# Performance work log

Hardware: AMD Instinct MI355X
Metric: run time of the kernel (lower is better)

## Reference

```python
import jax, jax.numpy as jnp
import numpy as np

B, S, D = 2, 2048, 1024
H, DH = 16, 64  # n_heads, d_head; D == H*DH
OUTPUT_SCALE = 1.0
EPS = 1e-08

def setup_inputs() -> dict:
    key = jax.random.key(0)
    k1, k2, k3 = jax.random.split(key, 3)
    x = jax.random.normal(k1, (B, S, D), dtype=jnp.float32)
    # causal-style mask would also work; use all-True [B,S,S] bool mask (True = attend)
    mask = jnp.tril(jnp.ones((S, S), dtype=bool))[None].repeat(B, axis=0)
    Wqkv = jax.random.normal(k2, (D, 3 * D), dtype=jnp.float32) * (1.0 / np.sqrt(D))
    Wo = jax.random.normal(k3, (D, D), dtype=jnp.float32) * (1.0 / np.sqrt(D))
    tau = jnp.full((H, 1, 1), float(DH) ** 0.5, dtype=jnp.float32)  # learned per-head temperature
    return {"x": x, "mask": mask, "Wqkv": Wqkv, "Wo": Wo, "tau": tau}

def reference(x, mask, Wqkv, Wo, tau):
    b, s, d = x.shape
    qkv = x @ Wqkv                                   # [B,S,3D]
    q, k, v = jnp.split(qkv, 3, axis=-1)
    # [B,S,D] -> [B,H,S,DH]
    q = q.reshape(b, s, H, DH).transpose(0, 2, 1, 3)
    k = k.reshape(b, s, H, DH).transpose(0, 2, 1, 3)
    v = v.reshape(b, s, H, DH).transpose(0, 2, 1, 3)
    # L2 normalize Q and K along head dim
    q = q / (jnp.linalg.norm(q, axis=-1, keepdims=True) + EPS)
    k = k / (jnp.linalg.norm(k, axis=-1, keepdims=True) + EPS)
    q = q * tau                                       # per-head learned temperature [H,1,1]
    logits = jnp.einsum('bhqd,bhkd->bhqk', q, k) / jnp.sqrt(jnp.float32(DH))
    m = mask if mask.ndim == 4 else mask[:, None, :, :]
    logits = jnp.where(m, logits, jnp.finfo(logits.dtype).min)
    w = jax.nn.softmax(logits, axis=-1)
    attn = jnp.einsum('bhqk,bhkd->bhqd', w, v)        # [B,H,S,DH]
    attn = attn.transpose(0, 2, 1, 3).reshape(b, s, d)
    return (attn @ Wo) * OUTPUT_SCALE
```

## Files before the change

### kernel.cpp

```cpp
#include <hip/hip_runtime.h>
#include <math.h>

#define BATCH 2
#define SEQ 2048
#define DMODEL 1024
#define NHEAD 16
#define DHEAD 64
#define QKV_COLS (3 * DMODEL)
#define EPS 1e-8f
#define LOG2E 1.44269504f

typedef short bf16x8 __attribute__((ext_vector_type(8)));
typedef float f32x4 __attribute__((ext_vector_type(4)));

static __device__ __forceinline__ unsigned short f2bf(float x) {
  unsigned u = __float_as_uint(x);
  u += 0x7fffu + ((u >> 16) & 1u);
  return (unsigned short)(u >> 16);
}

static __device__ __forceinline__ unsigned pkbf(float lo, float hi) {
  const unsigned ul = __float_as_uint(lo) + 0x8000u;
  const unsigned uh = __float_as_uint(hi) + 0x8000u;
  return __builtin_amdgcn_perm(uh, ul, 0x07060302);
}

static __device__ __forceinline__ void async_ld16(const unsigned short* g,
                                                  unsigned short* l) {
  __builtin_amdgcn_global_load_lds(
      (const __attribute__((address_space(1))) void*)g,
      (__attribute__((address_space(3))) void*)(unsigned int)(unsigned long long)l,
      16, 0, 0);
}

__global__ __launch_bounds__(256) void convert_x_kernel(
    const float* __restrict__ x, unsigned short* __restrict__ xb) {
  const size_t i = ((size_t)blockIdx.x * 256 + threadIdx.x) * 4;
  const float4 a = *(const float4*)(x + i);
  ushort4 r;
  r.x = f2bf(a.x); r.y = f2bf(a.y); r.z = f2bf(a.z); r.w = f2bf(a.w);
  *(ushort4*)(xb + i) = r;
}

__global__ __launch_bounds__(256) void transpose_w2_kernel(
    const float* __restrict__ W0, unsigned short* __restrict__ Wt0,
    const float* __restrict__ W1, unsigned short* __restrict__ Wt1) {
  __shared__ float tile[32][33];
  const int bx = blockIdx.x;
  const float* W;
  unsigned short* Wt;
  int N, n0;
  if (bx < 96) { W = W0; Wt = Wt0; N = QKV_COLS; n0 = bx * 32; }
  else         { W = W1; Wt = Wt1; N = DMODEL;   n0 = (bx - 96) * 32; }
  const int K = DMODEL;
  const int k0 = blockIdx.y * 32;
  const int tx = threadIdx.x, ty = threadIdx.y;
#pragma unroll
  for (int i = 0; i < 4; ++i)
    tile[ty + i * 8][tx] = W[(size_t)(k0 + ty + i * 8) * N + n0 + tx];
  __syncthreads();
#pragma unroll
  for (int i = 0; i < 4; ++i)
    Wt[(size_t)(n0 + ty + i * 8) * K + k0 + tx] = f2bf(tile[tx][ty + i * 8]);
}

__global__ __launch_bounds__(256) void sgemm_bf16_kernel(
    const unsigned short* __restrict__ A, const unsigned short* __restrict__ Bt,
    float* __restrict__ C, int M, int N, int K) {
  __shared__ unsigned short As[2][128 * 32];
  __shared__ unsigned short Bs[2][128 * 32];

  const int t = threadIdx.x;
  const int w = t >> 6;
  const int lane = t & 63;
  const int quad = lane >> 4;
  const int lr = lane & 15;
  const int wr = w >> 1, wc = w & 1;
  const int m0 = blockIdx.y * 128;
  const int n0 = blockIdx.x * 128;

  const int srow = w * 32 + (lane >> 2);
  const int scol = (lane & 3) * 8;
  const unsigned short* ga = A + (size_t)(m0 + srow) * K + scol;
  const unsigned short* gb = Bt + (size_t)(n0 + srow) * K + scol;

  auto stage = [&](int k0, int bb) {
#pragma unroll
    for (int i = 0; i < 2; ++i) {
      async_ld16(ga + (size_t)(i * 16) * K + k0, &As[bb][(w * 32 + i * 16) * 32]);
      async_ld16(gb + (size_t)(i * 16) * K + k0, &Bs[bb][(w * 32 + i * 16) * 32]);
    }
  };

  f32x4 acc[4][4];
  const f32x4 zero4 = {0.f, 0.f, 0.f, 0.f};
#pragma unroll
  for (int i = 0; i < 4; ++i)
#pragma unroll
    for (int j = 0; j < 4; ++j) acc[i][j] = zero4;

  stage(0, 0);
  int bb = 0;
  for (int k0 = 0; k0 < K; k0 += 32, bb ^= 1) {
    __syncthreads();
    if (k0 + 32 < K) stage(k0 + 32, bb ^ 1);

    bf16x8 af[4], bfr[4];
#pragma unroll
    for (int i = 0; i < 4; ++i)
      af[i] = *(const bf16x8*)&As[bb][(wr * 64 + i * 16 + lr) * 32 + quad * 8];
#pragma unroll
    for (int j = 0; j < 4; ++j)
      bfr[j] = *(const bf16x8*)&Bs[bb][(wc * 64 + j * 16 + lr) * 32 + quad * 8];
#pragma unroll
    for (int i = 0; i < 4; ++i)
#pragma unroll
      for (int j = 0; j < 4; ++j)
        acc[i][j] = __builtin_amdgcn_mfma_f32_16x16x32_bf16(af[i], bfr[j], acc[i][j], 0, 0, 0);
  }

#pragma unroll
  for (int i = 0; i < 4; ++i)
#pragma unroll
    for (int r = 0; r < 4; ++r) {
      float* c = C + (size_t)(m0 + wr * 64 + i * 16 + quad * 4 + r) * N + n0 + wc * 64 + lr;
#pragma unroll
      for (int j = 0; j < 4; ++j) c[j * 16] = acc[i][j][r];
    }
}

__global__ __launch_bounds__(256) void qkv_gemm_norm_kernel(
    const unsigned short* __restrict__ A, const unsigned short* __restrict__ Bt,
    const float* __restrict__ tau,
    unsigned short* __restrict__ Qh, unsigned short* __restrict__ Kh,
    unsigned short* __restrict__ Vh) {
  __shared__ unsigned short As[2][128 * 32];
  __shared__ unsigned short Bs[2][128 * 32];

  const int K = DMODEL, N = QKV_COLS;
  const int t = threadIdx.x;
  const int w = t >> 6;
  const int lane = t & 63;
  const int quad = lane >> 4;
  const int lr = lane & 15;
  const int wr = w >> 1, wc = w & 1;
  const int m0 = blockIdx.y * 128;
  const int n0 = blockIdx.x * 128;

  const int srow = w * 32 + (lane >> 2);
  const int scol = (lane & 3) * 8;
  const unsigned short* ga = A + (size_t)(m0 + srow) * K + scol;
  const unsigned short* gb = Bt + (size_t)(n0 + srow) * K + scol;

  auto stage = [&](int k0, int bb) {
#pragma unroll
    for (int i = 0; i < 2; ++i) {
      async_ld16(ga + (size_t)(i * 16) * K + k0, &As[bb][(w * 32 + i * 16) * 32]);
      async_ld16(gb + (size_t)(i * 16) * K + k0, &Bs[bb][(w * 32 + i * 16) * 32]);
    }
  };

  f32x4 acc[4][4];
  const f32x4 zero4 = {0.f, 0.f, 0.f, 0.f};
#pragma unroll
  for (int i = 0; i < 4; ++i)
#pragma unroll
    for (int j = 0; j < 4; ++j) acc[i][j] = zero4;

  stage(0, 0);
  int bb = 0;
  for (int k0 = 0; k0 < K; k0 += 32, bb ^= 1) {
    __syncthreads();
    if (k0 + 32 < K) stage(k0 + 32, bb ^ 1);

    bf16x8 af[4], bfr[4];
#pragma unroll
    for (int i = 0; i < 4; ++i)
      af[i] = *(const bf16x8*)&As[bb][(wr * 64 + i * 16 + lr) * 32 + quad * 8];
#pragma unroll
    for (int j = 0; j < 4; ++j)
      bfr[j] = *(const bf16x8*)&Bs[bb][(wc * 64 + j * 16 + lr) * 32 + quad * 8];
#pragma unroll
    for (int i = 0; i < 4; ++i)
#pragma unroll
      for (int j = 0; j < 4; ++j)
        acc[i][j] = __builtin_amdgcn_mfma_f32_16x16x32_bf16(af[i], bfr[j], acc[i][j], 0, 0, 0);
  }

  const int col0 = n0 + wc * 64;
  const int which = col0 >> 10;
  const int h = (col0 & 1023) >> 6;
  const float tsc = tau[h] * 0.125f * LOG2E;
  unsigned short* dst = (which == 0) ? Qh : (which == 1) ? Kh : Vh;

#pragma unroll
  for (int i = 0; i < 4; ++i)
#pragma unroll
    for (int r = 0; r < 4; ++r) {
      const int s = m0 + wr * 64 + i * 16 + quad * 4 + r;
      unsigned short* ar =
          dst + (((size_t)((s >> 11) * NHEAD + h)) * SEQ + (s & 2047)) * DHEAD;
      float scale;
      if (which == 2) {
        scale = 1.0f;
      } else {
        float ss = 0.f;
#pragma unroll
        for (int j = 0; j < 4; ++j) ss += acc[i][j][r] * acc[i][j][r];
        ss += __shfl_xor(ss, 1, 16);
        ss += __shfl_xor(ss, 2, 16);
        ss += __shfl_xor(ss, 4, 16);
        ss += __shfl_xor(ss, 8, 16);
        scale = 1.0f / (sqrtf(ss) + EPS);
        if (which == 0) scale *= tsc;
      }
#pragma unroll
      for (int j = 0; j < 4; ++j) ar[j * 16 + lr] = f2bf(acc[i][j][r] * scale);
    }
}

__global__ __launch_bounds__(256) void vtrans_kernel(
    const unsigned short* __restrict__ Vh, unsigned short* __restrict__ Vt) {
  __shared__ unsigned short tile[64][72];
  const int bh = blockIdx.x;
  const int s0 = blockIdx.y * 64;
  const int t = threadIdx.x;
  const int sr = t >> 2;
  const int dc = (t & 3) * 16;
  const unsigned short* src = Vh + ((size_t)bh * SEQ + s0 + sr) * DHEAD + dc;
  *(bf16x8*)&tile[sr][dc]     = *(const bf16x8*)(src);
  *(bf16x8*)&tile[sr][dc + 8] = *(const bf16x8*)(src + 8);
  __syncthreads();
  const int dr = t >> 2;
  const int sc = (t & 3) * 16;
  unsigned short buf[16];
#pragma unroll
  for (int i = 0; i < 16; ++i) buf[i] = tile[sc + i][dr];
  unsigned short* dst = Vt + ((size_t)bh * DHEAD + dr) * SEQ + s0 + sc;
  *(bf16x8*)dst       = *(const bf16x8*)buf;
  *(bf16x8*)(dst + 8) = *(const bf16x8*)(buf + 8);
}

#define PLS 72

__global__ __launch_bounds__(256, 2) void attn_kernel(
    const unsigned short* __restrict__ Qh, const unsigned short* __restrict__ Kh,
    const unsigned short* __restrict__ Vt, unsigned short* __restrict__ attnb) {
  __shared__ unsigned short Ks[2][2][64 * 32];
  __shared__ unsigned short Vs[2][2][64 * 32];
  __shared__ unsigned short Pl[4][16 * PLS];

  const int idx = blockIdx.x;
  const int bh = idx & 31;
  const int i = idx >> 5;
  const int qA = 31 - i, qB = i;
  const int b = bh >> 4;
  const int h = bh & 15;
  const int t = threadIdx.x;
  const int w = t >> 6;
  const int lane = t & 63;
  const int quad = lane >> 4;
  const int lr = lane & 15;

  const unsigned short* Qp = Qh + (size_t)bh * SEQ * DHEAD;
  const unsigned short* Kp = Kh + (size_t)bh * SEQ * DHEAD;
  const unsigned short* Vp = Vt + (size_t)bh * DHEAD * SEQ;
  unsigned short* Pw = &Pl[w][0];

  const int srow = lane >> 2;
  const int scol = (lane & 3) * 8;
  const int f0 = w * 4;

  auto stage = [&](int k0, int bb) {
#pragma unroll
    for (int ii = 0; ii < 4; ++ii) {
      const int fi = f0 + ii;
      if (fi < 8) {
        const int hh = fi >> 2, seg = fi & 3;
        async_ld16(Kp + (size_t)(k0 + seg * 16 + srow) * DHEAD + hh * 32 + scol,
                   &Ks[bb][hh][seg * 512]);
      } else {
        const int g = fi - 8;
        const int cc = g >> 2, seg = g & 3;
        async_ld16(Vp + (size_t)(seg * 16 + srow) * SEQ + k0 + cc * 32 + scol,
                   &Vs[bb][cc][seg * 512]);
      }
    }
  };

  const f32x4 zero4 = {0.f, 0.f, 0.f, 0.f};
  f32x4 o[4];
  o[0] = o[1] = o[2] = o[3] = zero4;
  float l_ = 0.f;

#define STEP(aq0_, aq1_, qb_, k0_, bb_, msk_)                                 \
  do {                                                                        \
    f32x4 c[4];                                                               \
    _Pragma("unroll")                                                         \
    for (int kt = 0; kt < 4; ++kt) {                                          \
      const bf16x8 kf0 = *(const bf16x8*)&Ks[bb_][0][(kt * 16 + lr) * 32 + quad * 8]; \
      const bf16x8 kf1 = *(const bf16x8*)&Ks[bb_][1][(kt * 16 + lr) * 32 + quad * 8]; \
      f32x4 tt = __builtin_amdgcn_mfma_f32_16x16x32_bf16(kf0, aq0_, zero4, 0, 0, 0);  \
      c[kt] = __builtin_amdgcn_mfma_f32_16x16x32_bf16(kf1, aq1_, tt, 0, 0, 0);        \
    }                                                                         \
    float ps = 0.f;                                                           \
    if (msk_) {                                                               \
      const int qrow = (qb_) + lr;                                            \
      _Pragma("unroll")                                                       \
      for (int kt = 0; kt < 4; ++kt) {                                        \
        float p[4];                                                           \
        _Pragma("unroll")                                                     \
        for (int r = 0; r < 4; ++r) {                                         \
          const int key = (k0_) + kt * 16 + quad * 4 + r;                     \
          p[r] = (key <= qrow) ? exp2f(c[kt][r]) : 0.f;                       \
          ps += p[r];                                                         \
        }                                                                     \
        const unsigned lo = pkbf(p[0], p[1]);                                 \
        const unsigned hi = pkbf(p[2], p[3]);                                 \
        *(unsigned long long*)&Pw[lr * PLS + kt * 16 + quad * 4] =            \
            ((unsigned long long)hi << 32) | lo;                              \
      }                                                                       \
    } else {                                                                  \
      _Pragma("unroll")                                                       \
      for (int kt = 0; kt < 4; ++kt) {                                        \
        float p[4];                                                           \
        _Pragma("unroll")                                                     \
        for (int r = 0; r < 4; ++r) {                                         \
          p[r] = exp2f(c[kt][r]);                                             \
          ps += p[r];                                                         \
        }                                                                     \
        const unsigned lo = pkbf(p[0], p[1]);                                 \
        const unsigned hi = pkbf(p[2], p[3]);                                 \
        *(unsigned long long*)&Pw[lr * PLS + kt * 16 + quad * 4] =            \
            ((unsigned long long)hi << 32) | lo;                              \
      }                                                                       \
    }                                                                         \
    l_ += ps;                                                                 \
    _Pragma("unroll")                                                         \
    for (int c2 = 0; c2 < 2; ++c2) {                                          \
      const bf16x8 pa = *(const bf16x8*)&Pw[lr * PLS + c2 * 32 + quad * 8];   \
      _Pragma("unroll")                                                       \
      for (int nt = 0; nt < 4; ++nt) {                                        \
        const bf16x8 vb = *(const bf16x8*)&Vs[bb_][c2][(nt * 16 + lr) * 32 + quad * 8]; \
        o[nt] = __builtin_amdgcn_mfma_f32_16x16x32_bf16(pa, vb, o[nt], 0, 0, 0);        \
      }                                                                       \
    }                                                                         \
  } while (0)

  auto epilogue = [&](int qbt) {
    float lt = l_;
    lt += __shfl_xor(lt, 16, 64);
    lt += __shfl_xor(lt, 32, 64);
    const float inv = 1.0f / lt;
#pragma unroll
    for (int r = 0; r < 4; ++r) {
      const float invr = __shfl(inv, quad * 4 + r, 16);
      unsigned short* ar =
          attnb + ((size_t)(b * SEQ + qbt + quad * 4 + r)) * DMODEL + h * DHEAD;
#pragma unroll
      for (int nt = 0; nt < 4; ++nt) ar[nt * 16 + lr] = f2bf(o[nt][r] * invr);
    }
  };

  const int qbA = qA * 64 + w * 16;
  const int qbB = qB * 64 + w * 16;
  const unsigned short* qrA = Qp + (size_t)(qbA + lr) * DHEAD;
  const unsigned short* qrB = Qp + (size_t)(qbB + lr) * DHEAD;
  const bf16x8 aqA0 = *(const bf16x8*)(qrA + quad * 8);
  const bf16x8 aqA1 = *(const bf16x8*)(qrA + 32 + quad * 8);
  const bf16x8 aqB0 = *(const bf16x8*)(qrB + quad * 8);
  const bf16x8 aqB1 = *(const bf16x8*)(qrB + 32 + quad * 8);

  const int kendA = qA * 64;
  const int kendB = qB * 64;

  stage(0, 0);
  int bb = 0;

  for (int k0 = 0; k0 <= kendA; k0 += 64, bb ^= 1) {
    __syncthreads();
    stage(k0 < kendA ? k0 + 64 : 0, bb ^ 1);
    STEP(aqA0, aqA1, qbA, k0, bb, (k0 == kendA));
  }
  epilogue(qbA);
  o[0] = o[1] = o[2] = o[3] = zero4;
  l_ = 0.f;

  for (int k0 = 0; k0 <= kendB; k0 += 64, bb ^= 1) {
    __syncthreads();
    if (k0 < kendB) stage(k0 + 64, bb ^ 1);
    STEP(aqB0, aqB1, qbB, k0, bb, (k0 == kendB));
  }
  epilogue(qbB);
#undef STEP
}

extern "C" void kernel_launch(void* const* d_in, const int* in_sizes, int n_in,
                              void* d_out, int out_size, void* d_ws, size_t ws_size,
                              hipStream_t stream) {
  const float* x    = (const float*)d_in[0];
  const float* Wqkv = (const float*)d_in[2];
  const float* Wo   = (const float*)d_in[3];
  const float* tau  = (const float*)d_in[4];
  float* out = (float*)d_out;

  unsigned short* attnb = (unsigned short*)d_ws;
  unsigned short* Qh = attnb + (size_t)BATCH * SEQ * DMODEL;
  unsigned short* Kh = Qh + (size_t)BATCH * NHEAD * SEQ * DHEAD;
  unsigned short* Vh = Kh + (size_t)BATCH * NHEAD * SEQ * DHEAD;
  unsigned short* Xb = Vh + (size_t)BATCH * NHEAD * SEQ * DHEAD;
  unsigned short* Wqkv_t = Xb + (size_t)BATCH * SEQ * DMODEL;
  unsigned short* Wo_t = Wqkv_t + (size_t)DMODEL * QKV_COLS;
  unsigned short* Vt = Wo_t + (size_t)DMODEL * DMODEL;

  const int M = BATCH * SEQ;

  convert_x_kernel<<<(M * DMODEL) / (256 * 4), 256, 0, stream>>>(x, Xb);
  transpose_w2_kernel<<<dim3(128, 32), dim3(32, 8), 0, stream>>>(
      Wqkv, Wqkv_t, Wo, Wo_t);

  qkv_gemm_norm_kernel<<<dim3(QKV_COLS / 128, M / 128), 256, 0, stream>>>(
      Xb, Wqkv_t, tau, Qh, Kh, Vh);

  vtrans_kernel<<<dim3(BATCH * NHEAD, SEQ / 64), 256, 0, stream>>>(Vh, Vt);

  attn_kernel<<<dim3(512), 256, 0, stream>>>(Qh, Kh, Vt, attnb);

  sgemm_bf16_kernel<<<dim3(DMODEL / 128, M / 128), 256, 0, stream>>>(
      attnb, Wo_t, out, M, DMODEL, DMODEL);
}
```

Before: 209.3 us.

## Split attention blocks per query tile, swizzle LDS, pass P via permlane swaps

The attention kernel now launches one block per 64-row query tile (1024 blocks) instead of pairing a long and a short tile per block. It orders tiles so heavy and light ones interleave, and raises launch bounds to 4 blocks per CU. The K/V LDS tiles become unified 64x64 buffers with an XOR swizzle to avoid bank conflicts. The P tile is rearranged into MFMA operand layout with v_permlane32/16_swap in registers instead of a round-trip through LDS, and s_setprio is raised around the MFMA sections. The intent is better occupancy and load balance plus fewer LDS transactions, at the cost of relying on the hardware scheduler to balance uneven causal tiles.

```diff
diff --git a/kernel.cpp b/kernel.cpp
--- a/kernel.cpp
+++ b/kernel.cpp
@@ -241,19 +241,17 @@
   *(bf16x8*)(dst + 8) = *(const bf16x8*)(buf + 8);
 }
 
-#define PLS 72
-
-__global__ __launch_bounds__(256, 2) void attn_kernel(
+__global__ __launch_bounds__(256, 4) void attn_kernel(
     const unsigned short* __restrict__ Qh, const unsigned short* __restrict__ Kh,
     const unsigned short* __restrict__ Vt, unsigned short* __restrict__ attnb) {
-  __shared__ unsigned short Ks[2][2][64 * 32];
-  __shared__ unsigned short Vs[2][2][64 * 32];
-  __shared__ unsigned short Pl[4][16 * PLS];
+  __shared__ unsigned short Ks[2][64 * 64];
+  __shared__ unsigned short Vs[2][64 * 64];
 
   const int idx = blockIdx.x;
   const int bh = idx & 31;
-  const int i = idx >> 5;
-  const int qA = 31 - i, qB = i;
+  const int i2 = idx >> 5;
+  const int seg = i2 >> 3, G = i2 & 7;
+  const int qb = (seg == 0) ? 31 - G : (seg == 1) ? G : (seg == 2) ? 23 - G : 8 + G;
   const int b = bh >> 4;
   const int h = bh & 15;
   const int t = threadIdx.x;
@@ -261,14 +259,14 @@
   const int lane = t & 63;
   const int quad = lane >> 4;
   const int lr = lane & 15;
+  const int sw = lr & 7;
 
   const unsigned short* Qp = Qh + (size_t)bh * SEQ * DHEAD;
   const unsigned short* Kp = Kh + (size_t)bh * SEQ * DHEAD;
   const unsigned short* Vp = Vt + (size_t)bh * DHEAD * SEQ;
-  unsigned short* Pw = &Pl[w][0];
-
-  const int srow = lane >> 2;
-  const int scol = (lane & 3) * 8;
+
+  const int rrow = lane >> 3;
+  const int swc = ((lane & 7) ^ rrow) * 8;
   const int f0 = w * 4;
 
   auto stage = [&](int k0, int bb) {
@@ -276,14 +274,12 @@
     for (int ii = 0; ii < 4; ++ii) {
       const int fi = f0 + ii;
       if (fi < 8) {
-        const int hh = fi >> 2, seg = fi & 3;
-        async_ld16(Kp + (size_t)(k0 + seg * 16 + srow) * DHEAD + hh * 32 + scol,
-                   &Ks[bb][hh][seg * 512]);
+        async_ld16(Kp + (size_t)(k0 + fi * 8 + rrow) * DHEAD + swc,
+                   &Ks[bb][fi * 512]);
       } else {
         const int g = fi - 8;
-        const int cc = g >> 2, seg = g & 3;
-        async_ld16(Vp + (size_t)(seg * 16 + srow) * SEQ + k0 + cc * 32 + scol,
-                   &Vs[bb][cc][seg * 512]);
+        async_ld16(Vp + (size_t)(g * 8 + rrow) * SEQ + k0 + swc,
+                   &Vs[bb][g * 512]);
       }
     }
   };
@@ -293,106 +289,98 @@
   o[0] = o[1] = o[2] = o[3] = zero4;
   float l_ = 0.f;
 
-#define STEP(aq0_, aq1_, qb_, k0_, bb_, msk_)                                 \
-  do {                                                                        \
-    f32x4 c[4];                                                               \
-    _Pragma("unroll")                                                         \
-    for (int kt = 0; kt < 4; ++kt) {                                          \
-      const bf16x8 kf0 = *(const bf16x8*)&Ks[bb_][0][(kt * 16 + lr) * 32 + quad * 8]; \
-      const bf16x8 kf1 = *(const bf16x8*)&Ks[bb_][1][(kt * 16 + lr) * 32 + quad * 8]; \
-      f32x4 tt = __builtin_amdgcn_mfma_f32_16x16x32_bf16(kf0, aq0_, zero4, 0, 0, 0);  \
-      c[kt] = __builtin_amdgcn_mfma_f32_16x16x32_bf16(kf1, aq1_, tt, 0, 0, 0);        \
-    }                                                                         \
-    float ps = 0.f;                                                           \
-    if (msk_) {                                                               \
-      const int qrow = (qb_) + lr;                                            \
-      _Pragma("unroll")                                                       \
-      for (int kt = 0; kt < 4; ++kt) {                                        \
-        float p[4];                                                           \
-        _Pragma("unroll")                                                     \
-        for (int r = 0; r < 4; ++r) {                                         \
-          const int key = (k0_) + kt * 16 + quad * 4 + r;                     \
-          p[r] = (key <= qrow) ? exp2f(c[kt][r]) : 0.f;                       \
-          ps += p[r];                                                         \
-        }                                                                     \
-        const unsigned lo = pkbf(p[0], p[1]);                                 \
-        const unsigned hi = pkbf(p[2], p[3]);                                 \
-        *(unsigned long long*)&Pw[lr * PLS + kt * 16 + quad * 4] =            \
-            ((unsigned long long)hi << 32) | lo;                              \
-      }                                                                       \
-    } else {                                                                  \
-      _Pragma("unroll")                                                       \
-      for (int kt = 0; kt < 4; ++kt) {                                        \
-        float p[4];                                                           \
-        _Pragma("unroll")                                                     \
-        for (int r = 0; r < 4; ++r) {                                         \
-          p[r] = exp2f(c[kt][r]);                                             \
-          ps += p[r];                                                         \
-        }                                                                     \
-        const unsigned lo = pkbf(p[0], p[1]);                                 \
-        const unsigned hi = pkbf(p[2], p[3]);                                 \
-        *(unsigned long long*)&Pw[lr * PLS + kt * 16 + quad * 4] =            \
-            ((unsigned long long)hi << 32) | lo;                              \
-      }                                                                       \
-    }                                                                         \
-    l_ += ps;                                                                 \
-    _Pragma("unroll")                                                         \
-    for (int c2 = 0; c2 < 2; ++c2) {                                          \
-      const bf16x8 pa = *(const bf16x8*)&Pw[lr * PLS + c2 * 32 + quad * 8];   \
-      _Pragma("unroll")                                                       \
-      for (int nt = 0; nt < 4; ++nt) {                                        \
-        const bf16x8 vb = *(const bf16x8*)&Vs[bb_][c2][(nt * 16 + lr) * 32 + quad * 8]; \
-        o[nt] = __builtin_amdgcn_mfma_f32_16x16x32_bf16(pa, vb, o[nt], 0, 0, 0);        \
-      }                                                                       \
-    }                                                                         \
-  } while (0)
-
-  auto epilogue = [&](int qbt) {
-    float lt = l_;
-    lt += __shfl_xor(lt, 16, 64);
-    lt += __shfl_xor(lt, 32, 64);
-    const float inv = 1.0f / lt;
-#pragma unroll
-    for (int r = 0; r < 4; ++r) {
-      const float invr = __shfl(inv, quad * 4 + r, 16);
-      unsigned short* ar =
-          attnb + ((size_t)(b * SEQ + qbt + quad * 4 + r)) * DMODEL + h * DHEAD;
-#pragma unroll
-      for (int nt = 0; nt < 4; ++nt) ar[nt * 16 + lr] = f2bf(o[nt][r] * invr);
-    }
-  };
-
-  const int qbA = qA * 64 + w * 16;
-  const int qbB = qB * 64 + w * 16;
-  const unsigned short* qrA = Qp + (size_t)(qbA + lr) * DHEAD;
-  const unsigned short* qrB = Qp + (size_t)(qbB + lr) * DHEAD;
-  const bf16x8 aqA0 = *(const bf16x8*)(qrA + quad * 8);
-  const bf16x8 aqA1 = *(const bf16x8*)(qrA + 32 + quad * 8);
-  const bf16x8 aqB0 = *(const bf16x8*)(qrB + quad * 8);
-  const bf16x8 aqB1 = *(const bf16x8*)(qrB + 32 + quad * 8);
-
-  const int kendA = qA * 64;
-  const int kendB = qB * 64;
+  const int q0 = qb * 64 + w * 16;
+  const unsigned short* qr = Qp + (size_t)(q0 + lr) * DHEAD;
+  const bf16x8 aq0 = *(const bf16x8*)(qr + quad * 8);
+  const bf16x8 aq1 = *(const bf16x8*)(qr + 32 + quad * 8);
+  const int qrow = q0 + lr;
+
+  const int kend = qb * 64;
 
   stage(0, 0);
   int bb = 0;
 
-  for (int k0 = 0; k0 <= kendA; k0 += 64, bb ^= 1) {
+  for (int k0 = 0; k0 <= kend; k0 += 64, bb ^= 1) {
     __syncthreads();
-    stage(k0 < kendA ? k0 + 64 : 0, bb ^ 1);
-    STEP(aqA0, aqA1, qbA, k0, bb, (k0 == kendA));
+    if (k0 < kend) stage(k0 + 64, bb ^ 1);
+
+    f32x4 c[4];
+    __builtin_amdgcn_s_setprio(1);
+#pragma unroll
+    for (int kt = 0; kt < 4; ++kt) {
+      const bf16x8 kf0 =
+          *(const bf16x8*)&Ks[bb][(kt * 16 + lr) * 64 + ((quad ^ sw) * 8)];
+      const bf16x8 kf1 =
+          *(const bf16x8*)&Ks[bb][(kt * 16 + lr) * 64 + (((4 | quad) ^ sw) * 8)];
+      f32x4 tt = __builtin_amdgcn_mfma_f32_16x16x32_bf16(kf0, aq0, zero4, 0, 0, 0);
+      c[kt] = __builtin_amdgcn_mfma_f32_16x16x32_bf16(kf1, aq1, tt, 0, 0, 0);
+    }
+    __builtin_amdgcn_s_setprio(0);
+
+    unsigned plo[4], phi[4];
+    float ps = 0.f;
+    if (k0 == kend) {
+#pragma unroll
+      for (int kt = 0; kt < 4; ++kt) {
+        float p[4];
+#pragma unroll
+        for (int r = 0; r < 4; ++r) {
+          const int key = k0 + kt * 16 + quad * 4 + r;
+          p[r] = (key <= qrow) ? exp2f(c[kt][r]) : 0.f;
+          ps += p[r];
+        }
+        plo[kt] = pkbf(p[0], p[1]);
+        phi[kt] = pkbf(p[2], p[3]);
+      }
+    } else {
+#pragma unroll
+      for (int kt = 0; kt < 4; ++kt) {
+        float p[4];
+#pragma unroll
+        for (int r = 0; r < 4; ++r) {
+          p[r] = exp2f(c[kt][r]);
+          ps += p[r];
+        }
+        plo[kt] = pkbf(p[0], p[1]);
+        phi[kt] = pkbf(p[2], p[3]);
+      }
+    }
+    l_ += ps;
+
+#pragma unroll
+    for (int c2 = 0; c2 < 2; ++c2) {
+      unsigned aLo = plo[2 * c2],     aHi = phi[2 * c2];
+      unsigned bLo = plo[2 * c2 + 1], bHi = phi[2 * c2 + 1];
+      asm("v_permlane32_swap_b32 %0, %1" : "+v"(aLo), "+v"(bLo));
+      asm("v_permlane32_swap_b32 %0, %1" : "+v"(aHi), "+v"(bHi));
+      asm("v_permlane16_swap_b32 %0, %1" : "+v"(aLo), "+v"(bLo));
+      asm("v_permlane16_swap_b32 %0, %1" : "+v"(aHi), "+v"(bHi));
+      union { unsigned u[4]; bf16x8 v; } pk;
+      pk.u[0] = aLo; pk.u[1] = aHi; pk.u[2] = bLo; pk.u[3] = bHi;
+      const bf16x8 pa = pk.v;
+      __builtin_amdgcn_s_setprio(1);
+#pragma unroll
+      for (int nt = 0; nt < 4; ++nt) {
+        const bf16x8 vb = *(const bf16x8*)&Vs[bb][(nt * 16 + lr) * 64 +
+                                                  (((c2 * 4 + quad) ^ sw) * 8)];
+        o[nt] = __builtin_amdgcn_mfma_f32_16x16x32_bf16(pa, vb, o[nt], 0, 0, 0);
+      }
+      __builtin_amdgcn_s_setprio(0);
+    }
   }
-  epilogue(qbA);
-  o[0] = o[1] = o[2] = o[3] = zero4;
-  l_ = 0.f;
-
-  for (int k0 = 0; k0 <= kendB; k0 += 64, bb ^= 1) {
-    __syncthreads();
-    if (k0 < kendB) stage(k0 + 64, bb ^ 1);
-    STEP(aqB0, aqB1, qbB, k0, bb, (k0 == kendB));
+
+  float lt = l_;
+  lt += __shfl_xor(lt, 16, 64);
+  lt += __shfl_xor(lt, 32, 64);
+  const float inv = 1.0f / lt;
+#pragma unroll
+  for (int r = 0; r < 4; ++r) {
+    const float invr = __shfl(inv, quad * 4 + r, 16);
+    unsigned short* ar =
+        attnb + ((size_t)(b * SEQ + q0 + quad * 4 + r)) * DMODEL + h * DHEAD;
+#pragma unroll
+    for (int nt = 0; nt < 4; ++nt) ar[nt * 16 + lr] = f2bf(o[nt][r] * invr);
   }
-  epilogue(qbB);
-#undef STEP
 }
 
 extern "C" void kernel_launch(void* const* d_in, const int* in_sizes, int n_in,
@@ -424,7 +412,7 @@
 
   vtrans_kernel<<<dim3(BATCH * NHEAD, SEQ / 64), 256, 0, stream>>>(Vh, Vt);
 
-  attn_kernel<<<dim3(512), 256, 0, stream>>>(Qh, Kh, Vt, attnb);
+  attn_kernel<<<dim3(1024), 256, 0, stream>>>(Qh, Kh, Vt, attnb);
 
   sgemm_bf16_kernel<<<dim3(DMODEL / 128, M / 128), 256, 0, stream>>>(
       attnb, Wo_t, out, M, DMODEL, DMODEL);
```

Measured after the change: 199.7 us. 1.05x faster.
